# Kernel tuning notes

Hardware: AMD Instinct MI355X
Metric: run time of the kernel (lower is better)

The kernel has to match this reference:

```python
import jax, jax.numpy as jnp
import numpy as np


def _make_dplr(N):
    # HiPPO-NPLR -> diagonalized (p, q, lambda), matching _make_p_q_lambda
    idx = np.arange(1, N + 1)
    hippo = np.where(
        idx[:, None] > idx[None, :],
        np.sqrt(2.0 * idx[:, None] + 1.0) * np.sqrt(2.0 * idx[None, :] + 1.0),
        np.where(idx[:, None] == idx[None, :], idx[:, None] + 1.0, 0.0),
    )
    p = 0.5 * np.sqrt(2.0 * idx + 1.0)
    q = 2.0 * p
    S = -hippo + p[:, None] * q[None, :]
    lam, V = np.linalg.eig(S)
    Vc = V.conj().T
    return Vc @ p.astype(np.complex128), Vc @ q.conj().astype(np.complex128), lam


def _ri(x):
    # complex -> [..., 2] float32 (torch.view_as_real layout)
    return np.stack([x.real, x.imag], axis=-1).astype(np.float32)


def setup_inputs() -> dict:
    D_MODEL, N, L_MAX, BATCH = 512, 64, 2048, 16
    key = jax.random.key(0)
    k_u, k_B, k_Ct, k_step = jax.random.split(key, 4)
    p, q, lam = _make_dplr(N)
    std = float(np.sqrt(2.0 / (D_MODEL + N)))  # xavier_normal gain=1
    B_ri = jax.random.normal(k_B, (D_MODEL, N, 2), dtype=jnp.float32) * (std / np.sqrt(2.0))
    Ct_ri = jax.random.normal(k_Ct, (D_MODEL, N, 2), dtype=jnp.float32) * (std / np.sqrt(2.0))
    dt_min, dt_max = 1e-3, 1e-1
    log_step = (jax.random.uniform(k_step, (D_MODEL,), dtype=jnp.float32)
                * float(np.log(dt_max) - np.log(dt_min)) + float(np.log(dt_min)))
    u = jax.random.normal(k_u, (BATCH, L_MAX, D_MODEL), dtype=jnp.float32)
    return {
        'u': u,
        'p_ri': jnp.asarray(_ri(p)),
        'q_ri': jnp.asarray(_ri(q)),
        'lam_ri': jnp.asarray(_ri(lam)),
        'B_ri': B_ri,
        'Ct_ri': Ct_ri,
        'D': jnp.ones((1, 1, D_MODEL), jnp.float32),
        'log_step': log_step,
    }


def _to_c(x):
    return jax.lax.complex(x[..., 0], x[..., 1])


def reference(u, p_ri, q_ri, lam_ri, B_ri, Ct_ri, D, log_step):
    l_max = u.shape[1]
    p, q, lam = _to_c(p_ri), _to_c(q_ri), _to_c(lam_ri)
    B, Ct = _to_c(B_ri), _to_c(Ct_ri)
    # roots of unity omega_l
    omega = jnp.exp((2j * np.pi / l_max) * jnp.arange(l_max)).astype(jnp.complex64)
    step = jnp.exp(log_step)
    g = jnp.outer(2.0 / step, (1.0 - omega) / (1.0 + omega))   # [d, L] complex
    c = 2.0 / (1.0 + omega)                                    # [L]
    # fused Cauchy kernel: one reciprocal tensor shared by all four dots
    r = 1.0 / (g[:, :, None] - lam[None, None, :])             # [d, L, n]
    a0, a1, b0, b1 = Ct.conj(), q.conj(), B, p
    k00 = jnp.einsum('dn,dln->dl', a0 * b0, r)
    k01 = jnp.einsum('dn,dln->dl', a0 * b1, r)
    k10 = jnp.einsum('dn,dln->dl', a1 * b0, r)
    k11 = jnp.einsum('n,dln->dl', a1 * b1, r)
    at_roots = c * (k00 - k01 * k10 / (1.0 + k11))             # [d, L]
    out = jnp.fft.ifft(at_roots, n=l_max, axis=-1)
    # ifft reordering: [0, L-1, L-2, ..., 1]
    order = jnp.concatenate([jnp.zeros((1,), jnp.int32), jnp.arange(l_max - 1, 0, -1, dtype=jnp.int32)])
    K = out[:, order].real[None]                               # [1, d, L]
    # non-circular (linear) convolution via length-2L FFT
    ud = jnp.fft.rfft(jnp.pad(u, ((0, 0), (0, l_max), (0, 0))), axis=1)   # [B, L+1, d]
    Kd = jnp.fft.rfft(jnp.pad(K, ((0, 0), (0, 0), (0, l_max))), axis=-1)  # [1, d, L+1]
    y = jnp.fft.irfft(jnp.swapaxes(ud, -2, -1) * Kd, axis=-1)[..., :l_max]
    return jnp.swapaxes(y, -2, -1) + D * u
```

## Files before the change

### kernel.cpp

```cpp
#include <hip/hip_runtime.h>

#define LMAX   2048
#define NFFT   4096
#define DMODEL 512
#define NSTATE 64
#define NBATCH 16
#define PI_D   3.14159265358979323846
#define NT_U   512
#define NT_K   512


__device__ __forceinline__ int swz(int a) { return a ^ ((a >> 5) & 31); }

__device__ __forceinline__ float2 cmul(float2 a, float2 b) {
  return make_float2(a.x*b.x - a.y*b.y, a.x*b.y + a.y*b.x);
}

__device__ __forceinline__ float2 twget(const float2* tw, int idx) {
  float2 w = tw[idx & 2047];
  if (idx & 2048) { w.x = -w.x; w.y = -w.y; }
  return w;
}

template<int LOGN, bool INV, int NT>
__device__ float2* fft_lds(float2* src, float2* dst, const float2* tw, int tid) {
  constexpr int N = 1 << LOGN;
  constexpr int NS8 = LOGN / 3;
  constexpr int TSH = 12 - LOGN;
  const float r2 = 0.70710678118654752f;
  int s = 1;
  #pragma unroll
  for (int st = 0; st < NS8; ++st) {
    __syncthreads();
    for (int i = tid; i < (N >> 3); i += NT) {
      const int q  = i & (s - 1);
      const int ps = i - q;
      float2 x[8];
      #pragma unroll
      for (int k = 0; k < 8; ++k) x[k] = src[swz(i + k * (N >> 3))];
      float2 E0,E1,E2,E3,O0,O1,O2,O3;
      {
        float2 u0 = make_float2(x[0].x+x[4].x, x[0].y+x[4].y);
        float2 v0 = make_float2(x[0].x-x[4].x, x[0].y-x[4].y);
        float2 u1 = make_float2(x[2].x+x[6].x, x[2].y+x[6].y);
        float2 v1 = make_float2(x[2].x-x[6].x, x[2].y-x[6].y);
        E0 = make_float2(u0.x+u1.x, u0.y+u1.y);
        E2 = make_float2(u0.x-u1.x, u0.y-u1.y);
        if (!INV) { E1 = make_float2(v0.x+v1.y, v0.y-v1.x); E3 = make_float2(v0.x-v1.y, v0.y+v1.x); }
        else      { E1 = make_float2(v0.x-v1.y, v0.y+v1.x); E3 = make_float2(v0.x+v1.y, v0.y-v1.x); }
      }
      {
        float2 u0 = make_float2(x[1].x+x[5].x, x[1].y+x[5].y);
        float2 v0 = make_float2(x[1].x-x[5].x, x[1].y-x[5].y);
        float2 u1 = make_float2(x[3].x+x[7].x, x[3].y+x[7].y);
        float2 v1 = make_float2(x[3].x-x[7].x, x[3].y-x[7].y);
        O0 = make_float2(u0.x+u1.x, u0.y+u1.y);
        O2 = make_float2(u0.x-u1.x, u0.y-u1.y);
        if (!INV) { O1 = make_float2(v0.x+v1.y, v0.y-v1.x); O3 = make_float2(v0.x-v1.y, v0.y+v1.x); }
        else      { O1 = make_float2(v0.x-v1.y, v0.y+v1.x); O3 = make_float2(v0.x+v1.y, v0.y-v1.x); }
      }
      float2 o1 = (!INV) ? make_float2((O1.x+O1.y)*r2, (O1.y-O1.x)*r2)
                         : make_float2((O1.x-O1.y)*r2, (O1.y+O1.x)*r2);
      float2 o2 = (!INV) ? make_float2(O2.y, -O2.x) : make_float2(-O2.y, O2.x);
      float2 o3 = (!INV) ? make_float2((O3.y-O3.x)*r2, -(O3.x+O3.y)*r2)
                         : make_float2(-(O3.x+O3.y)*r2, (O3.x-O3.y)*r2);
      float2 y[8];
      y[0] = make_float2(E0.x+O0.x, E0.y+O0.y);
      y[4] = make_float2(E0.x-O0.x, E0.y-O0.y);
      y[1] = make_float2(E1.x+o1.x, E1.y+o1.y);
      y[5] = make_float2(E1.x-o1.x, E1.y-o1.y);
      y[2] = make_float2(E2.x+o2.x, E2.y+o2.y);
      y[6] = make_float2(E2.x-o2.x, E2.y-o2.y);
      y[3] = make_float2(E3.x+o3.x, E3.y+o3.y);
      y[7] = make_float2(E3.x-o3.x, E3.y-o3.y);
      const int idx1  = ps << TSH;
      const int obase = q + (ps << 3);
      dst[swz(obase)] = y[0];
      #pragma unroll
      for (int j = 1; j < 8; ++j) {
        float2 w = twget(tw, j * idx1);
        if (INV) w.y = -w.y;
        dst[swz(obase + j * s)] = cmul(w, y[j]);
      }
    }
    s <<= 3;
    float2* t = src; src = dst; dst = t;
  }
  if constexpr (LOGN % 3 == 2) {
    __syncthreads();
    for (int i = tid; i < (N >> 2); i += NT) {
      const int q  = i & (s - 1);
      const int ps = i - q;
      float2 x0 = src[swz(i)];
      float2 x1 = src[swz(i + (N >> 2))];
      float2 x2 = src[swz(i + (N >> 1))];
      float2 x3 = src[swz(i + 3 * (N >> 2))];
      float2 u0 = make_float2(x0.x+x2.x, x0.y+x2.y), v0 = make_float2(x0.x-x2.x, x0.y-x2.y);
      float2 u1 = make_float2(x1.x+x3.x, x1.y+x3.y), v1 = make_float2(x1.x-x3.x, x1.y-x3.y);
      float2 y0 = make_float2(u0.x+u1.x, u0.y+u1.y);
      float2 y2 = make_float2(u0.x-u1.x, u0.y-u1.y);
      float2 y1, y3;
      if (!INV) { y1 = make_float2(v0.x+v1.y, v0.y-v1.x); y3 = make_float2(v0.x-v1.y, v0.y+v1.x); }
      else      { y1 = make_float2(v0.x-v1.y, v0.y+v1.x); y3 = make_float2(v0.x+v1.y, v0.y-v1.x); }
      const int idx1  = ps << TSH;
      const int obase = q + (ps << 2);
      float2 w1 = twget(tw, idx1), w2 = twget(tw, 2*idx1), w3 = twget(tw, 3*idx1);
      if (INV) { w1.y=-w1.y; w2.y=-w2.y; w3.y=-w3.y; }
      dst[swz(obase)]         = y0;
      dst[swz(obase + s)]     = cmul(w1, y1);
      dst[swz(obase + 2*s)]   = cmul(w2, y2);
      dst[swz(obase + 3*s)]   = cmul(w3, y3);
    }
    float2* t = src; src = dst; dst = t;
  }
  __syncthreads();
  return src;
}

__global__ void twiddle_init(float2* tw) {
  int j = blockIdx.x * blockDim.x + threadIdx.x;
  if (j < NFFT/2) {
    double ang = -2.0 * PI_D * (double)j / (double)NFFT;
    double s, c;
    sincos(ang, &s, &c);
    tw[j] = make_float2((float)c, (float)s);
  }
}

__global__ __launch_bounds__(NT_K) void s4_kernel_K(
    const float* __restrict__ p_ri, const float* __restrict__ q_ri,
    const float* __restrict__ lam_ri, const float* __restrict__ B_ri,
    const float* __restrict__ Ct_ri, const float* __restrict__ log_step,
    const float2* __restrict__ twg, float2* __restrict__ Kd)
{
  __shared__ float2 A[NFFT];
  __shared__ float2 Bb[NFFT];
  __shared__ float2 tw[NFFT/2];
  const int d = blockIdx.x;
  const int tid = threadIdx.x;

  for (int j = tid; j < NFFT/2; j += NT_K) tw[j] = twg[j];

  float2* lam = Bb;
  float2* w00 = Bb + 64;
  float2* w01 = Bb + 128;
  float2* w10 = Bb + 192;
  float2* w11 = Bb + 256;
  if (tid < NSTATE) {
    const int n = tid;
    float2 la = make_float2(lam_ri[2*n], lam_ri[2*n+1]);
    float2 pp = make_float2(p_ri[2*n],  p_ri[2*n+1]);
    float2 qq = make_float2(q_ri[2*n],  q_ri[2*n+1]);
    float2 Bv = make_float2(B_ri[(d*NSTATE+n)*2],  B_ri[(d*NSTATE+n)*2+1]);
    float2 Cv = make_float2(Ct_ri[(d*NSTATE+n)*2], Ct_ri[(d*NSTATE+n)*2+1]);
    lam[n] = la;
    w00[n] = make_float2(Cv.x*Bv.x + Cv.y*Bv.y, Cv.x*Bv.y - Cv.y*Bv.x);
    w01[n] = make_float2(Cv.x*pp.x + Cv.y*pp.y, Cv.x*pp.y - Cv.y*pp.x);
    w10[n] = make_float2(qq.x*Bv.x + qq.y*Bv.y, qq.x*Bv.y - qq.y*Bv.x);
    w11[n] = make_float2(qq.x*pp.x + qq.y*pp.y, qq.x*pp.y - qq.y*pp.x);
  }
  __syncthreads();

  const float two_over_step = 2.0f / expf(log_step[d]);
  for (int l = tid; l < LMAX; l += NT_K) {
    float theta = (float)(2.0 * PI_D / (double)LMAX) * (float)l;
    float si, co;
    sincosf(theta, &si, &co);
    float dx = 1.f + co, dy = si;
    float inv = 1.0f / (dx*dx + dy*dy);
    float2 c = make_float2(2.f*dx*inv, -2.f*dy*inv);
    float nx = 1.f - co, ny = -si;
    float2 g = make_float2(two_over_step * (nx*dx + ny*dy) * inv,
                           two_over_step * (ny*dx - nx*dy) * inv);
    float2 k00 = {0,0}, k01 = {0,0}, k10 = {0,0}, k11 = {0,0};
    #pragma unroll 8
    for (int n = 0; n < NSTATE; ++n) {
      float2 la = lam[n];
      float rr = g.x - la.x, ri = g.y - la.y;
      float rinv = 1.0f / (rr*rr + ri*ri);
      float2 r = make_float2(rr*rinv, -ri*rinv);
      float2 a;
      a = w00[n]; k00.x += a.x*r.x - a.y*r.y; k00.y += a.x*r.y + a.y*r.x;
      a = w01[n]; k01.x += a.x*r.x - a.y*r.y; k01.y += a.x*r.y + a.y*r.x;
      a = w10[n]; k10.x += a.x*r.x - a.y*r.y; k10.y += a.x*r.y + a.y*r.x;
      a = w11[n]; k11.x += a.x*r.x - a.y*r.y; k11.y += a.x*r.y + a.y*r.x;
    }
    float2 s1 = make_float2(1.f + k11.x, k11.y);
    float sinv = 1.0f / (s1.x*s1.x + s1.y*s1.y);
    float2 t = cmul(k01, k10);
    float2 tdiv = make_float2((t.x*s1.x + t.y*s1.y)*sinv, (t.y*s1.x - t.x*s1.y)*sinv);
    A[swz(l)] = cmul(c, make_float2(k00.x - tdiv.x, k00.y - tdiv.y));
  }

  float2* res = fft_lds<11, false, NT_K>(A, Bb, tw, tid);
  for (int k = tid; k < NFFT; k += NT_K) {
    float kr = (k < LMAX) ? res[swz(k)].x * (1.0f / LMAX) : 0.0f;
    Bb[swz(k)] = make_float2(kr, 0.f);
  }
  float2* res2 = fft_lds<12, false, NT_K>(Bb, A, tw, tid);
  for (int f = tid; f < NFFT; f += NT_K)
    Kd[(size_t)d * NFFT + f] = res2[swz(f)];
}

__global__ __launch_bounds__(NT_U) void s4_kernel_U(
    const float* __restrict__ u, const float* __restrict__ Dp,
    const float2* __restrict__ twg, const float2* __restrict__ Kd,
    float* __restrict__ out)
{
  __shared__ float2 A[NFFT];
  __shared__ float2 Bb[NFFT];
  __shared__ float2 tw[NFFT/2];
  const int bxr = blockIdx.x;
  const int dp  = (bxr & 7) * 32 + (bxr >> 3);
  const int b   = blockIdx.y;
  const int d0  = dp * 2;
  const int tid = threadIdx.x;

  for (int j = tid; j < NFFT/2; j += NT_U) tw[j] = twg[j];

  float2 ur[4];
  const float* ubase = u + ((size_t)b * LMAX) * DMODEL + d0;
  #pragma unroll
  for (int k = 0; k < 4; ++k) {
    const int l = tid + NT_U * k;
    float2 v = *(const float2*)(ubase + (size_t)l * DMODEL);
    ur[k] = v;
    A[swz(l)] = v;
  }
  #pragma unroll
  for (int k = 4; k < 8; ++k) A[swz(tid + NT_U * k)] = make_float2(0.f, 0.f);

  float2* Z = fft_lds<12, false, NT_U>(A, Bb, tw, tid);

  const float2* K0 = Kd + (size_t)d0 * NFFT;
  const float2* K1 = K0 + NFFT;
  #pragma unroll
  for (int k = 0; k < 8; ++k) {
    const int f = tid + NT_U * k;
    float2 zf = Z[swz(f)];
    float2 zr = Z[swz((NFFT - f) & (NFFT - 1))];
    float2 u0 = make_float2(0.5f*(zf.x + zr.x), 0.5f*(zf.y - zr.y));
    float2 du = make_float2(zf.x - zr.x, zf.y + zr.y);
    float2 u1 = make_float2(0.5f*du.y, -0.5f*du.x);
    float2 y0 = cmul(u0, K0[f]);
    float2 y1 = cmul(u1, K1[f]);
    Bb[swz(f)] = make_float2(y0.x - y1.y, y0.y + y1.x);
  }

  float2* W = fft_lds<12, true, NT_U>(Bb, A, tw, tid);

  const float D0 = Dp[d0], D1 = Dp[d0 + 1];
  float* obase = out + ((size_t)b * LMAX) * DMODEL + d0;
  const float scale = 1.0f / NFFT;
  #pragma unroll
  for (int k = 0; k < 4; ++k) {
    const int l = tid + NT_U * k;
    float2 w = W[swz(l)];
    float2 o = make_float2(w.x*scale + D0*ur[k].x, w.y*scale + D1*ur[k].y);
    *(float2*)(obase + (size_t)l * DMODEL) = o;
  }
}

extern "C" void kernel_launch(void* const* d_in, const int* in_sizes, int n_in,
                              void* d_out, int out_size, void* d_ws, size_t ws_size,
                              hipStream_t stream) {
  const float* u        = (const float*)d_in[0];
  const float* p_ri     = (const float*)d_in[1];
  const float* q_ri     = (const float*)d_in[2];
  const float* lam_ri   = (const float*)d_in[3];
  const float* B_ri     = (const float*)d_in[4];
  const float* Ct_ri    = (const float*)d_in[5];
  const float* Dp       = (const float*)d_in[6];
  const float* log_step = (const float*)d_in[7];
  float* out = (float*)d_out;

  float2* tw = (float2*)d_ws;
  float2* Kd = (float2*)((char*)d_ws + (NFFT/2) * sizeof(float2));

  twiddle_init<<<8, 256, 0, stream>>>(tw);
  s4_kernel_K<<<DMODEL, NT_K, 0, stream>>>(p_ri, q_ri, lam_ri, B_ri, Ct_ri,
                                           log_step, tw, Kd);
  s4_kernel_U<<<dim3(DMODEL/2, NBATCH), NT_U, 0, stream>>>(u, Dp, tw, Kd, out);
}
```

Measured before the change: 337.8 us.

## Rewrite S4 pipeline with in-place register FFTs and packed half-spectrum kernel

Replaces the ping-pong LDS FFT with in-place radix-8 FFTs that keep each butterfly in registers, use an XOR-folded LDS layout and read a global twiddle table with no per-block LDS copy. LDS use per block is halved. The K computation is split into a Cauchy+DIF-2048 kernel and a second kernel that FFTs two channels at once and stores a packed half-spectrum. The convolution then processes only half the frequencies via Hermitian symmetry, writing conjugate pairs directly. It also uses hardware approximate reciprocals, trading some accuracy for fewer instructions, and adds a kernel launch plus workspace traffic.

```diff
diff --git a/kernel.cpp b/kernel.cpp
--- a/kernel.cpp
+++ b/kernel.cpp
@@ -5,121 +5,233 @@
 #define DMODEL 512
 #define NSTATE 64
 #define NBATCH 16
+#define NT     512
 #define PI_D   3.14159265358979323846
-#define NT_U   512
-#define NT_K   512
-
-
-__device__ __forceinline__ int swz(int a) { return a ^ ((a >> 5) & 31); }
-
+#define REC_STRIDE 2050
+
+
+__device__ __forceinline__ int fold(int a) { return a ^ ((a>>3)&7) ^ ((a>>6)&7); }
+__device__ __forceinline__ int rev12(int t) {
+  return ((t&7)<<9) | (((t>>3)&7)<<6) | (((t>>6)&7)<<3) | ((t>>9)&7);
+}
+__device__ __forceinline__ int rev11(int t) {
+  return ((t&7)<<8) | (((t>>3)&7)<<5) | (((t>>6)&7)<<2) | ((t>>9)&3);
+}
 __device__ __forceinline__ float2 cmul(float2 a, float2 b) {
   return make_float2(a.x*b.x - a.y*b.y, a.x*b.y + a.y*b.x);
 }
-
-__device__ __forceinline__ float2 twget(const float2* tw, int idx) {
-  float2 w = tw[idx & 2047];
-  if (idx & 2048) { w.x = -w.x; w.y = -w.y; }
-  return w;
-}
-
-template<int LOGN, bool INV, int NT>
-__device__ float2* fft_lds(float2* src, float2* dst, const float2* tw, int tid) {
-  constexpr int N = 1 << LOGN;
-  constexpr int NS8 = LOGN / 3;
-  constexpr int TSH = 12 - LOGN;
+__device__ __forceinline__ float2 cmulc(float2 a, float2 b) {
+  return make_float2(a.x*b.x + a.y*b.y, a.y*b.x - a.x*b.y);
+}
+__device__ __forceinline__ float rcpf(float x) { return __builtin_amdgcn_rcpf(x); }
+
+template<bool INV>
+__device__ __forceinline__ void bf8(float2 x[8]) {
   const float r2 = 0.70710678118654752f;
-  int s = 1;
-  #pragma unroll
-  for (int st = 0; st < NS8; ++st) {
-    __syncthreads();
-    for (int i = tid; i < (N >> 3); i += NT) {
-      const int q  = i & (s - 1);
-      const int ps = i - q;
-      float2 x[8];
-      #pragma unroll
-      for (int k = 0; k < 8; ++k) x[k] = src[swz(i + k * (N >> 3))];
-      float2 E0,E1,E2,E3,O0,O1,O2,O3;
-      {
-        float2 u0 = make_float2(x[0].x+x[4].x, x[0].y+x[4].y);
-        float2 v0 = make_float2(x[0].x-x[4].x, x[0].y-x[4].y);
-        float2 u1 = make_float2(x[2].x+x[6].x, x[2].y+x[6].y);
-        float2 v1 = make_float2(x[2].x-x[6].x, x[2].y-x[6].y);
-        E0 = make_float2(u0.x+u1.x, u0.y+u1.y);
-        E2 = make_float2(u0.x-u1.x, u0.y-u1.y);
-        if (!INV) { E1 = make_float2(v0.x+v1.y, v0.y-v1.x); E3 = make_float2(v0.x-v1.y, v0.y+v1.x); }
-        else      { E1 = make_float2(v0.x-v1.y, v0.y+v1.x); E3 = make_float2(v0.x+v1.y, v0.y-v1.x); }
-      }
-      {
-        float2 u0 = make_float2(x[1].x+x[5].x, x[1].y+x[5].y);
-        float2 v0 = make_float2(x[1].x-x[5].x, x[1].y-x[5].y);
-        float2 u1 = make_float2(x[3].x+x[7].x, x[3].y+x[7].y);
-        float2 v1 = make_float2(x[3].x-x[7].x, x[3].y-x[7].y);
-        O0 = make_float2(u0.x+u1.x, u0.y+u1.y);
-        O2 = make_float2(u0.x-u1.x, u0.y-u1.y);
-        if (!INV) { O1 = make_float2(v0.x+v1.y, v0.y-v1.x); O3 = make_float2(v0.x-v1.y, v0.y+v1.x); }
-        else      { O1 = make_float2(v0.x-v1.y, v0.y+v1.x); O3 = make_float2(v0.x+v1.y, v0.y-v1.x); }
-      }
-      float2 o1 = (!INV) ? make_float2((O1.x+O1.y)*r2, (O1.y-O1.x)*r2)
-                         : make_float2((O1.x-O1.y)*r2, (O1.y+O1.x)*r2);
-      float2 o2 = (!INV) ? make_float2(O2.y, -O2.x) : make_float2(-O2.y, O2.x);
-      float2 o3 = (!INV) ? make_float2((O3.y-O3.x)*r2, -(O3.x+O3.y)*r2)
-                         : make_float2(-(O3.x+O3.y)*r2, (O3.x-O3.y)*r2);
-      float2 y[8];
-      y[0] = make_float2(E0.x+O0.x, E0.y+O0.y);
-      y[4] = make_float2(E0.x-O0.x, E0.y-O0.y);
-      y[1] = make_float2(E1.x+o1.x, E1.y+o1.y);
-      y[5] = make_float2(E1.x-o1.x, E1.y-o1.y);
-      y[2] = make_float2(E2.x+o2.x, E2.y+o2.y);
-      y[6] = make_float2(E2.x-o2.x, E2.y-o2.y);
-      y[3] = make_float2(E3.x+o3.x, E3.y+o3.y);
-      y[7] = make_float2(E3.x-o3.x, E3.y-o3.y);
-      const int idx1  = ps << TSH;
-      const int obase = q + (ps << 3);
-      dst[swz(obase)] = y[0];
-      #pragma unroll
-      for (int j = 1; j < 8; ++j) {
-        float2 w = twget(tw, j * idx1);
-        if (INV) w.y = -w.y;
-        dst[swz(obase + j * s)] = cmul(w, y[j]);
-      }
-    }
-    s <<= 3;
-    float2* t = src; src = dst; dst = t;
-  }
-  if constexpr (LOGN % 3 == 2) {
-    __syncthreads();
-    for (int i = tid; i < (N >> 2); i += NT) {
-      const int q  = i & (s - 1);
-      const int ps = i - q;
-      float2 x0 = src[swz(i)];
-      float2 x1 = src[swz(i + (N >> 2))];
-      float2 x2 = src[swz(i + (N >> 1))];
-      float2 x3 = src[swz(i + 3 * (N >> 2))];
-      float2 u0 = make_float2(x0.x+x2.x, x0.y+x2.y), v0 = make_float2(x0.x-x2.x, x0.y-x2.y);
-      float2 u1 = make_float2(x1.x+x3.x, x1.y+x3.y), v1 = make_float2(x1.x-x3.x, x1.y-x3.y);
-      float2 y0 = make_float2(u0.x+u1.x, u0.y+u1.y);
-      float2 y2 = make_float2(u0.x-u1.x, u0.y-u1.y);
-      float2 y1, y3;
-      if (!INV) { y1 = make_float2(v0.x+v1.y, v0.y-v1.x); y3 = make_float2(v0.x-v1.y, v0.y+v1.x); }
-      else      { y1 = make_float2(v0.x-v1.y, v0.y+v1.x); y3 = make_float2(v0.x+v1.y, v0.y-v1.x); }
-      const int idx1  = ps << TSH;
-      const int obase = q + (ps << 2);
-      float2 w1 = twget(tw, idx1), w2 = twget(tw, 2*idx1), w3 = twget(tw, 3*idx1);
-      if (INV) { w1.y=-w1.y; w2.y=-w2.y; w3.y=-w3.y; }
-      dst[swz(obase)]         = y0;
-      dst[swz(obase + s)]     = cmul(w1, y1);
-      dst[swz(obase + 2*s)]   = cmul(w2, y2);
-      dst[swz(obase + 3*s)]   = cmul(w3, y3);
-    }
-    float2* t = src; src = dst; dst = t;
-  }
-  __syncthreads();
-  return src;
+  float2 E0,E1,E2,E3,O0,O1,O2,O3;
+  {
+    float2 u0 = make_float2(x[0].x+x[4].x, x[0].y+x[4].y);
+    float2 v0 = make_float2(x[0].x-x[4].x, x[0].y-x[4].y);
+    float2 u1 = make_float2(x[2].x+x[6].x, x[2].y+x[6].y);
+    float2 v1 = make_float2(x[2].x-x[6].x, x[2].y-x[6].y);
+    E0 = make_float2(u0.x+u1.x, u0.y+u1.y);
+    E2 = make_float2(u0.x-u1.x, u0.y-u1.y);
+    if (!INV) { E1 = make_float2(v0.x+v1.y, v0.y-v1.x); E3 = make_float2(v0.x-v1.y, v0.y+v1.x); }
+    else      { E1 = make_float2(v0.x-v1.y, v0.y+v1.x); E3 = make_float2(v0.x+v1.y, v0.y-v1.x); }
+  }
+  {
+    float2 u0 = make_float2(x[1].x+x[5].x, x[1].y+x[5].y);
+    float2 v0 = make_float2(x[1].x-x[5].x, x[1].y-x[5].y);
+    float2 u1 = make_float2(x[3].x+x[7].x, x[3].y+x[7].y);
+    float2 v1 = make_float2(x[3].x-x[7].x, x[3].y-x[7].y);
+    O0 = make_float2(u0.x+u1.x, u0.y+u1.y);
+    O2 = make_float2(u0.x-u1.x, u0.y-u1.y);
+    if (!INV) { O1 = make_float2(v0.x+v1.y, v0.y-v1.x); O3 = make_float2(v0.x-v1.y, v0.y+v1.x); }
+    else      { O1 = make_float2(v0.x-v1.y, v0.y+v1.x); O3 = make_float2(v0.x+v1.y, v0.y-v1.x); }
+  }
+  float2 o1 = (!INV) ? make_float2((O1.x+O1.y)*r2, (O1.y-O1.x)*r2)
+                     : make_float2((O1.x-O1.y)*r2, (O1.y+O1.x)*r2);
+  float2 o2 = (!INV) ? make_float2(O2.y, -O2.x) : make_float2(-O2.y, O2.x);
+  float2 o3 = (!INV) ? make_float2((O3.y-O3.x)*r2, -(O3.x+O3.y)*r2)
+                     : make_float2(-(O3.x+O3.y)*r2, (O3.x-O3.y)*r2);
+  x[0] = make_float2(E0.x+O0.x, E0.y+O0.y);
+  x[4] = make_float2(E0.x-O0.x, E0.y-O0.y);
+  x[1] = make_float2(E1.x+o1.x, E1.y+o1.y);
+  x[5] = make_float2(E1.x-o1.x, E1.y-o1.y);
+  x[2] = make_float2(E2.x+o2.x, E2.y+o2.y);
+  x[6] = make_float2(E2.x-o2.x, E2.y-o2.y);
+  x[3] = make_float2(E3.x+o3.x, E3.y+o3.y);
+  x[7] = make_float2(E3.x-o3.x, E3.y-o3.y);
+}
+
+__device__ __forceinline__ void bf4(float2 x[4]) {
+  float2 u0 = make_float2(x[0].x+x[2].x, x[0].y+x[2].y);
+  float2 v0 = make_float2(x[0].x-x[2].x, x[0].y-x[2].y);
+  float2 u1 = make_float2(x[1].x+x[3].x, x[1].y+x[3].y);
+  float2 v1 = make_float2(x[1].x-x[3].x, x[1].y-x[3].y);
+  x[0] = make_float2(u0.x+u1.x, u0.y+u1.y);
+  x[2] = make_float2(u0.x-u1.x, u0.y-u1.y);
+  x[1] = make_float2(v0.x+v1.y, v0.y-v1.x);
+  x[3] = make_float2(v0.x-v1.y, v0.y+v1.x);
+}
+
+template<bool INV>
+__device__ void fft4096(float2* Z, const float2* __restrict__ tw, int tid) {
+  int ad[8]; float2 x[8];
+  if constexpr (!INV) {
+    __syncthreads();
+    {
+      const int p = tid;
+      const int xb = ((p>>3)&7) ^ ((p>>6)&7);
+      #pragma unroll
+      for (int k=0;k<8;k++){ ad[k] = (p + (k<<9)) ^ xb; x[k] = Z[ad[k]]; }
+      bf8<false>(x);
+      Z[ad[0]] = x[0];
+      #pragma unroll
+      for (int j=1;j<8;j++) Z[ad[j]] = cmul(tw[p*j], x[j]);
+    }
+    __syncthreads();
+    {
+      const int p = tid & 63, B = tid >> 6;
+      const int base = (B<<9) | p;
+      const int xb = (p>>3)&7;
+      #pragma unroll
+      for (int k=0;k<8;k++){ ad[k] = ((base | (k<<6)) ^ xb) ^ k; x[k] = Z[ad[k]]; }
+      bf8<false>(x);
+      Z[ad[0]] = x[0];
+      #pragma unroll
+      for (int j=1;j<8;j++) Z[ad[j]] = cmul(tw[(p*j)<<3], x[j]);
+    }
+    __syncthreads();
+    {
+      const int p = tid & 7, B = tid >> 3;
+      const int base = (B<<6) | p;
+      const int xb = B & 7;
+      #pragma unroll
+      for (int k=0;k<8;k++){ ad[k] = ((base | (k<<3)) ^ xb) ^ k; x[k] = Z[ad[k]]; }
+      bf8<false>(x);
+      Z[ad[0]] = x[0];
+      #pragma unroll
+      for (int j=1;j<8;j++) Z[ad[j]] = cmul(tw[(p*j)<<6], x[j]);
+    }
+    __syncthreads();
+    {
+      const int B = tid;
+      const int xb = (B&7) ^ ((B>>3)&7);
+      #pragma unroll
+      for (int k=0;k<8;k++){ ad[k] = (B<<3) | (k ^ xb); x[k] = Z[ad[k]]; }
+      bf8<false>(x);
+      #pragma unroll
+      for (int j=0;j<8;j++) Z[ad[j]] = x[j];
+    }
+    __syncthreads();
+  } else {
+    __syncthreads();
+    {
+      const int B = tid;
+      const int xb = (B&7) ^ ((B>>3)&7);
+      #pragma unroll
+      for (int k=0;k<8;k++){ ad[k] = (B<<3) | (k ^ xb); x[k] = Z[ad[k]]; }
+      bf8<true>(x);
+      #pragma unroll
+      for (int j=0;j<8;j++) Z[ad[j]] = x[j];
+    }
+    __syncthreads();
+    {
+      const int p = tid & 7, B = tid >> 3;
+      const int base = (B<<6) | p;
+      const int xb = B & 7;
+      #pragma unroll
+      for (int k=0;k<8;k++){ ad[k] = ((base | (k<<3)) ^ xb) ^ k; x[k] = Z[ad[k]]; }
+      #pragma unroll
+      for (int k=1;k<8;k++) x[k] = cmulc(x[k], tw[(p*k)<<6]);
+      bf8<true>(x);
+      #pragma unroll
+      for (int j=0;j<8;j++) Z[ad[j]] = x[j];
+    }
+    __syncthreads();
+    {
+      const int p = tid & 63, B = tid >> 6;
+      const int base = (B<<9) | p;
+      const int xb = (p>>3)&7;
+      #pragma unroll
+      for (int k=0;k<8;k++){ ad[k] = ((base | (k<<6)) ^ xb) ^ k; x[k] = Z[ad[k]]; }
+      #pragma unroll
+      for (int k=1;k<8;k++) x[k] = cmulc(x[k], tw[(p*k)<<3]);
+      bf8<true>(x);
+      #pragma unroll
+      for (int j=0;j<8;j++) Z[ad[j]] = x[j];
+    }
+    __syncthreads();
+    {
+      const int p = tid;
+      const int xb = ((p>>3)&7) ^ ((p>>6)&7);
+      #pragma unroll
+      for (int k=0;k<8;k++){ ad[k] = (p + (k<<9)) ^ xb; x[k] = Z[ad[k]]; }
+      #pragma unroll
+      for (int k=1;k<8;k++) x[k] = cmulc(x[k], tw[p*k]);
+      bf8<true>(x);
+      #pragma unroll
+      for (int j=0;j<8;j++) Z[ad[j]] = x[j];
+    }
+    __syncthreads();
+  }
+}
+
+__device__ void dif2048(float2* Z, const float2* __restrict__ tw, int tid) {
+  int ad[8]; float2 x[8];
+  __syncthreads();
+  if (tid < 256) {
+    const int p = tid;
+    const int xb = ((p>>3)&7) ^ ((p>>6)&3);
+    #pragma unroll
+    for (int k=0;k<8;k++){ ad[k] = ((p | (k<<8)) ^ xb) ^ ((k&1)<<2); x[k] = Z[ad[k]]; }
+    bf8<false>(x);
+    Z[ad[0]] = x[0];
+    #pragma unroll
+    for (int j=1;j<8;j++) Z[ad[j]] = cmul(tw[(p*j)<<1], x[j]);
+  }
+  __syncthreads();
+  if (tid < 256) {
+    const int p = tid & 31, B = tid >> 5;
+    const int base = (B<<8) | p;
+    const int xb = ((p>>3)&3) ^ ((B&1)<<2);
+    #pragma unroll
+    for (int k=0;k<8;k++){ ad[k] = ((base | (k<<5)) ^ xb) ^ (((k&1)<<2) | (k>>1)); x[k] = Z[ad[k]]; }
+    bf8<false>(x);
+    Z[ad[0]] = x[0];
+    #pragma unroll
+    for (int j=1;j<8;j++) Z[ad[j]] = cmul(tw[(p*j)<<4], x[j]);
+  }
+  __syncthreads();
+  if (tid < 256) {
+    const int p = tid & 3, B = tid >> 2;
+    const int base = (B<<5) | p;
+    const int xb = ((B&1)<<2) ^ ((B>>1)&7);
+    #pragma unroll
+    for (int k=0;k<8;k++){ ad[k] = ((base | (k<<2)) ^ xb) ^ (k>>1); x[k] = Z[ad[k]]; }
+    bf8<false>(x);
+    Z[ad[0]] = x[0];
+    #pragma unroll
+    for (int j=1;j<8;j++) Z[ad[j]] = cmul(tw[(p*j)<<7], x[j]);
+  }
+  __syncthreads();
+  {
+    const int B = tid;
+    const int xb = ((B>>1)&7) ^ ((B>>4)&7);
+    float2 y[4]; int a4[4];
+    #pragma unroll
+    for (int j=0;j<4;j++){ a4[j] = ((B<<2) | j) ^ xb; y[j] = Z[a4[j]]; }
+    bf4(y);
+    #pragma unroll
+    for (int j=0;j<4;j++) Z[a4[j]] = y[j];
+  }
+  __syncthreads();
 }
 
 __global__ void twiddle_init(float2* tw) {
   int j = blockIdx.x * blockDim.x + threadIdx.x;
-  if (j < NFFT/2) {
+  if (j < NFFT) {
     double ang = -2.0 * PI_D * (double)j / (double)NFFT;
     double s, c;
     sincos(ang, &s, &c);
@@ -127,25 +239,17 @@
   }
 }
 
-__global__ __launch_bounds__(NT_K) void s4_kernel_K(
+__global__ __launch_bounds__(NT) void s4_kernelA(
     const float* __restrict__ p_ri, const float* __restrict__ q_ri,
     const float* __restrict__ lam_ri, const float* __restrict__ B_ri,
     const float* __restrict__ Ct_ri, const float* __restrict__ log_step,
-    const float2* __restrict__ twg, float2* __restrict__ Kd)
+    const float2* __restrict__ tw, float* __restrict__ Ktime)
 {
-  __shared__ float2 A[NFFT];
-  __shared__ float2 Bb[NFFT];
-  __shared__ float2 tw[NFFT/2];
+  __shared__ float2 Z[2048 + 5*64];
+  float2* Wg = Z + 2048;
   const int d = blockIdx.x;
   const int tid = threadIdx.x;
 
-  for (int j = tid; j < NFFT/2; j += NT_K) tw[j] = twg[j];
-
-  float2* lam = Bb;
-  float2* w00 = Bb + 64;
-  float2* w01 = Bb + 128;
-  float2* w10 = Bb + 192;
-  float2* w11 = Bb + 256;
   if (tid < NSTATE) {
     const int n = tid;
     float2 la = make_float2(lam_ri[2*n], lam_ri[2*n+1]);
@@ -153,109 +257,155 @@
     float2 qq = make_float2(q_ri[2*n],  q_ri[2*n+1]);
     float2 Bv = make_float2(B_ri[(d*NSTATE+n)*2],  B_ri[(d*NSTATE+n)*2+1]);
     float2 Cv = make_float2(Ct_ri[(d*NSTATE+n)*2], Ct_ri[(d*NSTATE+n)*2+1]);
-    lam[n] = la;
-    w00[n] = make_float2(Cv.x*Bv.x + Cv.y*Bv.y, Cv.x*Bv.y - Cv.y*Bv.x);
-    w01[n] = make_float2(Cv.x*pp.x + Cv.y*pp.y, Cv.x*pp.y - Cv.y*pp.x);
-    w10[n] = make_float2(qq.x*Bv.x + qq.y*Bv.y, qq.x*Bv.y - qq.y*Bv.x);
-    w11[n] = make_float2(qq.x*pp.x + qq.y*pp.y, qq.x*pp.y - qq.y*pp.x);
-  }
-  __syncthreads();
-
-  const float two_over_step = 2.0f / expf(log_step[d]);
-  for (int l = tid; l < LMAX; l += NT_K) {
+    Wg[n] = la;
+    Wg[64 +n] = make_float2(Cv.x*Bv.x + Cv.y*Bv.y, Cv.x*Bv.y - Cv.y*Bv.x);
+    Wg[128+n] = make_float2(Cv.x*pp.x + Cv.y*pp.y, Cv.x*pp.y - Cv.y*pp.x);
+    Wg[192+n] = make_float2(qq.x*Bv.x + qq.y*Bv.y, qq.x*Bv.y - qq.y*Bv.x);
+    Wg[256+n] = make_float2(qq.x*pp.x + qq.y*pp.y, qq.x*pp.y - qq.y*pp.x);
+  }
+  __syncthreads();
+
+  const float tos = 2.0f * rcpf(expf(log_step[d]));
+  float2 g[4], cc[4];
+  #pragma unroll
+  for (int il=0; il<4; ++il) {
+    const int l = tid + (il<<9);
     float theta = (float)(2.0 * PI_D / (double)LMAX) * (float)l;
     float si, co;
     sincosf(theta, &si, &co);
     float dx = 1.f + co, dy = si;
-    float inv = 1.0f / (dx*dx + dy*dy);
-    float2 c = make_float2(2.f*dx*inv, -2.f*dy*inv);
+    float inv = rcpf(dx*dx + dy*dy);
+    cc[il] = make_float2(2.f*dx*inv, -2.f*dy*inv);
     float nx = 1.f - co, ny = -si;
-    float2 g = make_float2(two_over_step * (nx*dx + ny*dy) * inv,
-                           two_over_step * (ny*dx - nx*dy) * inv);
-    float2 k00 = {0,0}, k01 = {0,0}, k10 = {0,0}, k11 = {0,0};
-    #pragma unroll 8
-    for (int n = 0; n < NSTATE; ++n) {
-      float2 la = lam[n];
-      float rr = g.x - la.x, ri = g.y - la.y;
-      float rinv = 1.0f / (rr*rr + ri*ri);
-      float2 r = make_float2(rr*rinv, -ri*rinv);
-      float2 a;
-      a = w00[n]; k00.x += a.x*r.x - a.y*r.y; k00.y += a.x*r.y + a.y*r.x;
-      a = w01[n]; k01.x += a.x*r.x - a.y*r.y; k01.y += a.x*r.y + a.y*r.x;
-      a = w10[n]; k10.x += a.x*r.x - a.y*r.y; k10.y += a.x*r.y + a.y*r.x;
-      a = w11[n]; k11.x += a.x*r.x - a.y*r.y; k11.y += a.x*r.y + a.y*r.x;
-    }
-    float2 s1 = make_float2(1.f + k11.x, k11.y);
-    float sinv = 1.0f / (s1.x*s1.x + s1.y*s1.y);
-    float2 t = cmul(k01, k10);
+    g[il] = make_float2(tos*(nx*dx + ny*dy)*inv, tos*(ny*dx - nx*dy)*inv);
+  }
+  float2 a00[4], a01[4], a10[4], a11[4];
+  #pragma unroll
+  for (int il=0; il<4; ++il) { a00[il]=make_float2(0,0); a01[il]=make_float2(0,0);
+                               a10[il]=make_float2(0,0); a11[il]=make_float2(0,0); }
+  for (int nc = 0; nc < NSTATE; nc += 4) {
+    float2 la[4], w0[4], w1[4], w2[4], w3[4];
+    #pragma unroll
+    for (int j=0;j<4;j++) {
+      la[j] = Wg[nc+j];      w0[j] = Wg[64+nc+j];  w1[j] = Wg[128+nc+j];
+      w2[j] = Wg[192+nc+j];  w3[j] = Wg[256+nc+j];
+    }
+    #pragma unroll
+    for (int il=0; il<4; ++il) {
+      #pragma unroll
+      for (int j=0;j<4;j++) {
+        float rr = g[il].x - la[j].x, ri = g[il].y - la[j].y;
+        float rinv = rcpf(rr*rr + ri*ri);
+        float rx = rr*rinv, ry = -ri*rinv;
+        a00[il].x += w0[j].x*rx - w0[j].y*ry; a00[il].y += w0[j].x*ry + w0[j].y*rx;
+        a01[il].x += w1[j].x*rx - w1[j].y*ry; a01[il].y += w1[j].x*ry + w1[j].y*rx;
+        a10[il].x += w2[j].x*rx - w2[j].y*ry; a10[il].y += w2[j].x*ry + w2[j].y*rx;
+        a11[il].x += w3[j].x*rx - w3[j].y*ry; a11[il].y += w3[j].x*ry + w3[j].y*rx;
+      }
+    }
+  }
+  #pragma unroll
+  for (int il=0; il<4; ++il) {
+    const int l = tid + (il<<9);
+    float2 s1 = make_float2(1.f + a11[il].x, a11[il].y);
+    float sinv = rcpf(s1.x*s1.x + s1.y*s1.y);
+    float2 t = cmul(a01[il], a10[il]);
     float2 tdiv = make_float2((t.x*s1.x + t.y*s1.y)*sinv, (t.y*s1.x - t.x*s1.y)*sinv);
-    A[swz(l)] = cmul(c, make_float2(k00.x - tdiv.x, k00.y - tdiv.y));
-  }
-
-  float2* res = fft_lds<11, false, NT_K>(A, Bb, tw, tid);
-  for (int k = tid; k < NFFT; k += NT_K) {
-    float kr = (k < LMAX) ? res[swz(k)].x * (1.0f / LMAX) : 0.0f;
-    Bb[swz(k)] = make_float2(kr, 0.f);
-  }
-  float2* res2 = fft_lds<12, false, NT_K>(Bb, A, tw, tid);
-  for (int f = tid; f < NFFT; f += NT_K)
-    Kd[(size_t)d * NFFT + f] = res2[swz(f)];
-}
-
-__global__ __launch_bounds__(NT_U) void s4_kernel_U(
+    Z[fold(l)] = cmul(cc[il], make_float2(a00[il].x - tdiv.x, a00[il].y - tdiv.y));
+  }
+
+  dif2048(Z, tw, tid);
+
+  #pragma unroll
+  for (int il=0; il<4; ++il) {
+    const int kk = tid + (il<<9);
+    Ktime[(size_t)d * LMAX + kk] = Z[fold(rev11(kk))].x * (1.0f / LMAX);
+  }
+}
+
+__global__ __launch_bounds__(NT) void s4_kernelB(
+    const float* __restrict__ Ktime, const float2* __restrict__ tw,
+    float4* __restrict__ Kd)
+{
+  __shared__ float2 Z[NFFT];
+  const int dp = blockIdx.x;
+  const int tid = threadIdx.x;
+  const float* K0p = Ktime + (size_t)(2*dp) * LMAX;
+  const float* K1p = K0p + LMAX;
+  #pragma unroll
+  for (int il=0; il<4; ++il) {
+    const int kk = tid + (il<<9);
+    Z[fold(kk)] = make_float2(K0p[kk], K1p[kk]);
+    Z[fold(LMAX + kk)] = make_float2(0.f, 0.f);
+  }
+  fft4096<false>(Z, tw, tid);
+  float4* rec = Kd + (size_t)dp * REC_STRIDE;
+  #pragma unroll
+  for (int it=0; it<5; ++it) {
+    int t = tid + (it<<9);
+    if (it == 4) { if (tid != 0) break; t = 2048; }
+    const int j1 = fold(rev12(t));
+    const int j2 = fold(rev12((NFFT - t) & (NFFT-1)));
+    float2 zf = Z[j1], zr = Z[j2];
+    float k0x = 0.5f*(zf.x + zr.x), k0y = 0.5f*(zf.y - zr.y);
+    float dx = zf.x - zr.x, dy = zf.y + zr.y;
+    rec[t] = make_float4(k0x, k0y, 0.5f*dy, -0.5f*dx);
+  }
+}
+
+__global__ __launch_bounds__(NT) void s4_conv(
     const float* __restrict__ u, const float* __restrict__ Dp,
-    const float2* __restrict__ twg, const float2* __restrict__ Kd,
+    const float2* __restrict__ tw, const float4* __restrict__ Kd,
     float* __restrict__ out)
 {
-  __shared__ float2 A[NFFT];
-  __shared__ float2 Bb[NFFT];
-  __shared__ float2 tw[NFFT/2];
+  __shared__ float2 Z[NFFT];
   const int bxr = blockIdx.x;
   const int dp  = (bxr & 7) * 32 + (bxr >> 3);
   const int b   = blockIdx.y;
   const int d0  = dp * 2;
   const int tid = threadIdx.x;
 
-  for (int j = tid; j < NFFT/2; j += NT_U) tw[j] = twg[j];
-
   float2 ur[4];
   const float* ubase = u + ((size_t)b * LMAX) * DMODEL + d0;
   #pragma unroll
-  for (int k = 0; k < 4; ++k) {
-    const int l = tid + NT_U * k;
+  for (int k=0; k<4; ++k) {
+    const int l = tid + (k<<9);
     float2 v = *(const float2*)(ubase + (size_t)l * DMODEL);
     ur[k] = v;
-    A[swz(l)] = v;
-  }
-  #pragma unroll
-  for (int k = 4; k < 8; ++k) A[swz(tid + NT_U * k)] = make_float2(0.f, 0.f);
-
-  float2* Z = fft_lds<12, false, NT_U>(A, Bb, tw, tid);
-
-  const float2* K0 = Kd + (size_t)d0 * NFFT;
-  const float2* K1 = K0 + NFFT;
-  #pragma unroll
-  for (int k = 0; k < 8; ++k) {
-    const int f = tid + NT_U * k;
-    float2 zf = Z[swz(f)];
-    float2 zr = Z[swz((NFFT - f) & (NFFT - 1))];
+    Z[fold(l)] = v;
+    Z[fold(LMAX + l)] = make_float2(0.f, 0.f);
+  }
+
+  fft4096<false>(Z, tw, tid);
+
+  const float4* rec = Kd + (size_t)dp * REC_STRIDE;
+  #pragma unroll
+  for (int it=0; it<5; ++it) {
+    int t = tid + (it<<9);
+    if (it == 4) { if (tid != 0) break; t = 2048; }
+    const int j1 = fold(rev12(t));
+    const int j2 = fold(rev12((NFFT - t) & (NFFT-1)));
+    float2 zf = Z[j1], zr = Z[j2];
+    float4 r4 = rec[t];
+    float2 K0 = make_float2(r4.x, r4.y), K1 = make_float2(r4.z, r4.w);
     float2 u0 = make_float2(0.5f*(zf.x + zr.x), 0.5f*(zf.y - zr.y));
-    float2 du = make_float2(zf.x - zr.x, zf.y + zr.y);
-    float2 u1 = make_float2(0.5f*du.y, -0.5f*du.x);
-    float2 y0 = cmul(u0, K0[f]);
-    float2 y1 = cmul(u1, K1[f]);
-    Bb[swz(f)] = make_float2(y0.x - y1.y, y0.y + y1.x);
-  }
-
-  float2* W = fft_lds<12, true, NT_U>(Bb, A, tw, tid);
+    float du_x = zf.x - zr.x, du_y = zf.y + zr.y;
+    float2 u1 = make_float2(0.5f*du_y, -0.5f*du_x);
+    float2 P = cmul(u0, K0);
+    float2 Q = cmul(u1, K1);
+    Z[j1] = make_float2(P.x - Q.y, P.y + Q.x);
+    Z[j2] = make_float2(P.x + Q.y, Q.x - P.y);
+  }
+
+  fft4096<true>(Z, tw, tid);
 
   const float D0 = Dp[d0], D1 = Dp[d0 + 1];
   float* obase = out + ((size_t)b * LMAX) * DMODEL + d0;
   const float scale = 1.0f / NFFT;
   #pragma unroll
-  for (int k = 0; k < 4; ++k) {
-    const int l = tid + NT_U * k;
-    float2 w = W[swz(l)];
+  for (int k=0; k<4; ++k) {
+    const int l = tid + (k<<9);
+    float2 w = Z[fold(l)];
     float2 o = make_float2(w.x*scale + D0*ur[k].x, w.y*scale + D1*ur[k].y);
     *(float2*)(obase + (size_t)l * DMODEL) = o;
   }
@@ -274,11 +424,15 @@
   const float* log_step = (const float*)d_in[7];
   float* out = (float*)d_out;
 
-  float2* tw = (float2*)d_ws;
-  float2* Kd = (float2*)((char*)d_ws + (NFFT/2) * sizeof(float2));
-
-  twiddle_init<<<8, 256, 0, stream>>>(tw);
-  s4_kernel_K<<<DMODEL, NT_K, 0, stream>>>(p_ri, q_ri, lam_ri, B_ri, Ct_ri,
-                                           log_step, tw, Kd);
-  s4_kernel_U<<<dim3(DMODEL/2, NBATCH), NT_U, 0, stream>>>(u, Dp, tw, Kd, out);
-}
+  char* wsb = (char*)d_ws;
+  float2* tw    = (float2*)wsb;
+  float4* Kd    = (float4*)(wsb + NFFT * sizeof(float2));
+  float*  Ktime = (float*)(wsb + NFFT * sizeof(float2)
+                               + (size_t)256 * REC_STRIDE * sizeof(float4));
+
+  twiddle_init<<<16, 256, 0, stream>>>(tw);
+  s4_kernelA<<<DMODEL, NT, 0, stream>>>(p_ri, q_ri, lam_ri, B_ri, Ct_ri,
+                                        log_step, tw, Ktime);
+  s4_kernelB<<<DMODEL/2, NT, 0, stream>>>(Ktime, tw, Kd);
+  s4_conv<<<dim3(DMODEL/2, NBATCH), NT, 0, stream>>>(u, Dp, tw, Kd, out);
+}
```

After: 360.4 us. 6.7% more time.
